# Optimization experiments

Measured on AMD Instinct MI355X. Metric: run time of the kernel, lower is better.

The kernel has to match this reference:

```python
import jax, jax.numpy as jnp
import numpy as np

T, B, I, H, L = 512, 256, 128, 256, 2


def setup_inputs() -> dict:
    key = jax.random.key(0)
    ks = jax.random.split(key, 7)
    s = 0.05
    return {
        "x": jax.random.normal(ks[0], (T, B, I), jnp.float32),
        "state": jnp.zeros((L, B, H), jnp.float32),
        "Wi0": jax.random.normal(ks[1], (3 * H, I), jnp.float32) * s,
        "Wh0": jax.random.normal(ks[2], (3 * H, H), jnp.float32) * s,
        "Wn0": jax.random.normal(ks[3], (3 * H // 3, I), jnp.float32) * s,
        "Wi1": jax.random.normal(ks[4], (3 * H, H), jnp.float32) * s,
        "Wh1": jax.random.normal(ks[5], (3 * H, H), jnp.float32) * s,
        "Wn1": jax.random.normal(ks[6], (H, H), jnp.float32) * s,
    }


def _cell(x, h, Wi, Wh, Wn):
    # gates: [B, 3H]; only r, z chunks are used (third chunk discarded, as in source)
    gates = x @ Wi.T + h @ Wh.T
    hs = h.shape[-1]
    r = jax.nn.sigmoid(gates[..., :hs])
    z = jax.nn.sigmoid(gates[..., hs:2 * hs])
    n = jnp.tanh(x @ Wn.T + r * h)  # note: r gates h directly (nonstandard GRU)
    return (1 - z) * n + z * h


def reference(x, state, Wi0, Wh0, Wn0, Wi1, Wh1, Wn1):
    params = ((Wi0, Wh0, Wn0), (Wi1, Wh1, Wn1))

    def step(carry, xt):
        h0, h1 = carry
        h0 = _cell(xt, h0, *params[0])
        h1 = _cell(h0, h1, *params[1])
        return (h0, h1), h1

    (h0, h1), out = jax.lax.scan(step, (state[0], state[1]), x)
    h = jnp.stack([h0, h1])
    return out, h
```

## Files before the change

kernel.cpp:

```cpp
#include <hip/hip_runtime.h>

#define T_ 512
#define B_ 256
#define I_ 128
#define H_ 256
#define SPIN_MAX (1 << 18)

typedef unsigned short ushort_t;
typedef unsigned int uint_t;
typedef unsigned long long u64_t;
typedef __attribute__((ext_vector_type(8))) short short8;
typedef __attribute__((ext_vector_type(4))) float f32x4;

#define XG_OFF   0
#define H0R_OFF  786432
#define QA_OFF   1048576
#define QB_OFF   1572864
#define FL_OFF   1835008
#define N_FLAGS  2048

__device__ __forceinline__ ushort_t f2bf(float f) {
  unsigned int u = __float_as_uint(f);
  u += 0x7fffu + ((u >> 16) & 1u);
  return (ushort_t)(u >> 16);
}
__device__ __forceinline__ float bf2f(ushort_t u) {
  return __uint_as_float(((unsigned int)u) << 16);
}

__global__ void prep_kernel(uint_t* __restrict__ ws) {
  int i = blockIdx.x * 256 + threadIdx.x;
  if (i < N_FLAGS) ((int*)(ws + FL_OFF))[i] = 0;
}

struct frag2 { short8 h, m; };

__device__ __forceinline__ frag2 lda_x2(const float* base, int ldk, int kc, int lane) {
  const float* p = base + (size_t)(lane & 15) * ldk + kc * 32 + ((lane >> 4) << 3);
  f32x4 a = *(const f32x4*)p;
  f32x4 b = *(const f32x4*)(p + 4);
  float v[8] = {a[0], a[1], a[2], a[3], b[0], b[1], b[2], b[3]};
  frag2 r;
#pragma unroll
  for (int j = 0; j < 8; j++) {
    float f = v[j];
    ushort_t xx = f2bf(f); f -= bf2f(xx);
    ushort_t y = f2bf(f);
    r.h[j] = (short)xx; r.m[j] = (short)y;
  }
  return r;
}
__device__ __forceinline__ short8 ldw1(const float* base, int ldk, int row, int kc, int lane) {
  const float* p = base + (size_t)(row + (lane & 15)) * ldk + kc * 32 + ((lane >> 4) << 3);
  f32x4 a = *(const f32x4*)p;
  f32x4 b = *(const f32x4*)(p + 4);
  short8 r;
  r[0] = (short)f2bf(a[0]); r[1] = (short)f2bf(a[1]);
  r[2] = (short)f2bf(a[2]); r[3] = (short)f2bf(a[3]);
  r[4] = (short)f2bf(b[0]); r[5] = (short)f2bf(b[1]);
  r[6] = (short)f2bf(b[2]); r[7] = (short)f2bf(b[3]);
  return r;
}
__device__ __forceinline__ frag2 ld_packed(const uint_t* p) {
  const u64_t* qp = (const u64_t*)p;
  u64_t d0 = __hip_atomic_load(qp + 0, __ATOMIC_RELAXED, __HIP_MEMORY_SCOPE_AGENT);
  u64_t d1 = __hip_atomic_load(qp + 1, __ATOMIC_RELAXED, __HIP_MEMORY_SCOPE_AGENT);
  u64_t d2 = __hip_atomic_load(qp + 2, __ATOMIC_RELAXED, __HIP_MEMORY_SCOPE_AGENT);
  u64_t d3 = __hip_atomic_load(qp + 3, __ATOMIC_RELAXED, __HIP_MEMORY_SCOPE_AGENT);
  u64_t d[4] = {d0, d1, d2, d3};
  frag2 f;
#pragma unroll
  for (int j = 0; j < 4; j++) {
    uint_t lo = (uint_t)d[j];
    uint_t hi = (uint_t)(d[j] >> 32);
    f.h[2 * j]     = (short)(lo & 0xffffu); f.m[2 * j]     = (short)(lo >> 16);
    f.h[2 * j + 1] = (short)(hi & 0xffffu); f.m[2 * j + 1] = (short)(hi >> 16);
  }
  return f;
}
__device__ __forceinline__ float ldf32(const uint_t* p) {
  uint_t v = __hip_atomic_load(p, __ATOMIC_RELAXED, __HIP_MEMORY_SCOPE_AGENT);
  return __uint_as_float(v);
}
#define CFENCE() asm volatile("" ::: "memory")

__device__ __forceinline__ f32x4 mfma_(short8 a, short8 b, f32x4 c) {
  return __builtin_amdgcn_mfma_f32_16x16x32_bf16(a, b, c, 0, 0, 0);
}
__device__ __forceinline__ int lpoll(const int* p, int tgt, int act, int aborted) {
  if (aborted) return aborted;
  int n = 0;
  for (;;) {
    int ok = 1;
    if (act && tgt > 0)
      ok = (__hip_atomic_load(p, __ATOMIC_RELAXED, __HIP_MEMORY_SCOPE_AGENT) >= tgt);
    if (__all(ok)) return 0;
    if (++n > SPIN_MAX) return 1;
  }
}
__device__ __forceinline__ int lcheck(const int* p, int tgt, int act) {
  int ok = 1;
  if (act && tgt > 0)
    ok = (__hip_atomic_load(p, __ATOMIC_RELAXED, __HIP_MEMORY_SCOPE_AGENT) >= tgt);
  return __all(ok);
}
__device__ __forceinline__ void stflag(int* p, int v) {
  __hip_atomic_store(p, v, __ATOMIC_RELAXED, __HIP_MEMORY_SCOPE_AGENT);
}
__device__ __forceinline__ int get_xcc() {
  int x;
  asm volatile("s_getreg_b32 %0, hwreg(HW_REG_XCC_ID)" : "=s"(x));
  return x & 15;
}
__device__ __forceinline__ float cellpw_fast(float gr, float gz, float np, float h) {
  float r = __builtin_amdgcn_rcpf(1.0f + __builtin_amdgcn_exp2f(-1.44269504089f * gr));
  float z = __builtin_amdgcn_rcpf(1.0f + __builtin_amdgcn_exp2f(-1.44269504089f * gz));
  float a = np + r * h;
  float n = 1.0f - 2.0f * __builtin_amdgcn_rcpf(1.0f + __builtin_amdgcn_exp2f(2.88539008177f * a));
  return (1.0f - z) * n + z * h;
}

__global__ void __launch_bounds__(256, 1)
gru_main(const float* __restrict__ x,
         const float* __restrict__ Wi0, const float* __restrict__ Wh0, const float* __restrict__ Wn0,
         const float* __restrict__ Wi1, const float* __restrict__ Wh1, const float* __restrict__ Wn1,
         const float* __restrict__ state, float* __restrict__ out,
         uint_t* __restrict__ ws, int* __restrict__ unused_flags) {
  __shared__ ushort_t hp[2][2][16][264];
  __shared__ float hf[16][264];
  __shared__ int s_fast;

  const int tid = (int)threadIdx.x;
  const int lane = tid & 63;
  const int wv = tid >> 6;
  const int bid = (int)blockIdx.x;
  const int g = bid & 15;
  const int role = bid >> 4;
  const int gb = g * 16;
  const int c0 = wv * 64;
  const int arow = lane & 15;
  const int acol = (lane >> 4) << 3;
  const int q = lane >> 4;

  int* flags = (int*)(ws + FL_OFF);
  int* fg = flags + g * 32;
  uint_t* xgp = ws + XG_OFF + (size_t)g * 49152;
  uint_t* h0r = ws + H0R_OFF + (size_t)g * 16384;
  uint_t* qap = ws + QA_OFF + (size_t)g * 32768;
  uint_t* qbp = ws + QB_OFF + (size_t)g * 16384;

  if (tid == 0) {
    int myx = get_xcc();
    __hip_atomic_store(&flags[1024 + bid], myx, __ATOMIC_RELAXED, __HIP_MEMORY_SCOPE_AGENT);
    __threadfence();
    __hip_atomic_fetch_add(&flags[1536 + g * 16], 1, __ATOMIC_RELEASE, __HIP_MEMORY_SCOPE_AGENT);
    int n = 0, ab = 0;
    while (__hip_atomic_load(&flags[1536 + g * 16], __ATOMIC_RELAXED,
                             __HIP_MEMORY_SCOPE_AGENT) < 5) {
      if (++n > SPIN_MAX) { ab = 1; break; }
    }
    __threadfence();
    int f = ab ? 0 : 1;
    if (!ab) {
#pragma unroll
      for (int r = 0; r < 5; r++)
        f &= (__hip_atomic_load(&flags[1024 + r * 16 + g], __ATOMIC_RELAXED,
                                __HIP_MEMORY_SCOPE_AGENT) == myx);
    }
    s_fast = f;
  }

  if (role == 1 || role == 4) {
    const float* st = state + (role == 4 ? (size_t)B_ * H_ : 0);
#pragma unroll
    for (int j = 0; j < 4; j++)
#pragma unroll
      for (int e = 0; e < 4; e++) {
        int row = q * 4 + e, col = c0 + 16 * j + (lane & 15);
        float f = st[(size_t)(gb + row) * H_ + col];
        hf[row][col] = f;
        ushort_t hi = f2bf(f), mid = f2bf(f - bf2f(hi));
        hp[1][0][row][col] = hi;
        hp[1][1][row][col] = mid;
      }
  }
  __syncthreads();
  const int fast = s_fast;
  int aborted = 0, ready = 0;
  const f32x4 zz = {0.f, 0.f, 0.f, 0.f};

  if (role == 0) {
    short8 Wxr[4][4], Wxz[4][4], Wxn[4][4];
#pragma unroll
    for (int j = 0; j < 4; j++)
#pragma unroll
      for (int kc = 0; kc < 4; kc++) {
        Wxr[j][kc] = ldw1(Wi0, I_, c0 + 16 * j, kc, lane);
        Wxz[j][kc] = ldw1(Wi0, I_, 256 + c0 + 16 * j, kc, lane);
        Wxn[j][kc] = ldw1(Wn0, I_, c0 + 16 * j, kc, lane);
      }
    const int* wp = fg + 8;
    for (int t = 0; t < T_; t++) {
      if (!ready) aborted = lpoll(wp, t - 3, lane == 0, aborted);
      CFENCE();
      f32x4 ar[4] = {zz, zz, zz, zz}, az[4] = {zz, zz, zz, zz}, an[4] = {zz, zz, zz, zz};
      const float* xt = x + ((size_t)t * B_ + gb) * I_;
#pragma unroll
      for (int kc = 0; kc < 4; kc++) {
        frag2 a = lda_x2(xt, I_, kc, lane);
#pragma unroll
        for (int j = 0; j < 4; j++) {
          ar[j] = mfma_(a.h, Wxr[j][kc], ar[j]); ar[j] = mfma_(a.m, Wxr[j][kc], ar[j]);
          az[j] = mfma_(a.h, Wxz[j][kc], az[j]); az[j] = mfma_(a.m, Wxz[j][kc], az[j]);
          an[j] = mfma_(a.h, Wxn[j][kc], an[j]); an[j] = mfma_(a.m, Wxn[j][kc], an[j]);
        }
      }
      float* xs = (float*)(xgp + (size_t)(t & 3) * 12288);
#pragma unroll
      for (int j = 0; j < 4; j++)
#pragma unroll
        for (int e = 0; e < 4; e++) {
          int row = q * 4 + e, col = c0 + 16 * j + (lane & 15);
          xs[row * 768 + col] = ar[j][e];
          xs[row * 768 + 256 + col] = az[j][e];
          xs[row * 768 + 512 + col] = an[j][e];
        }
      asm volatile("s_waitcnt vmcnt(0)" ::: "memory");
      if (!fast) __threadfence();
      if (lane == 0) stflag(fg + wv, t + 1);
      ready = fast ? lcheck(wp, t - 2, lane == 0) : 0;
    }
  } else if (role == 1) {
    short8 Whr[4][8], Whz[4][8];
#pragma unroll
    for (int j = 0; j < 4; j++)
#pragma unroll
      for (int kc = 0; kc < 8; kc++) {
        Whr[j][kc] = ldw1(Wh0, H_, c0 + 16 * j, kc, lane);
        Whz[j][kc] = ldw1(Wh0, H_, 256 + c0 + 16 * j, kc, lane);
      }
    const int hact = lane < 12;
    const int* hpn = fg + ((lane < 4) ? lane : (lane < 8 ? 12 + (lane - 4) : 16 + (lane - 8)));
    for (int t = 0; t < T_; t++) {
      if (!ready) aborted = lpoll(hpn, (lane < 4) ? t + 1 : t - 3, hact, aborted);
      if (!fast) __threadfence();
      CFENCE();
      const uint_t* xs = xgp + (size_t)(t & 3) * 12288;
      float xr[4][4], xz[4][4], xn[4][4];
#pragma unroll
      for (int j = 0; j < 4; j++)
#pragma unroll
        for (int e = 0; e < 4; e++) {
          int row = q * 4 + e, col = c0 + 16 * j + (lane & 15);
          xr[j][e] = ldf32(xs + row * 768 + col);
          xz[j][e] = ldf32(xs + row * 768 + 256 + col);
          xn[j][e] = ldf32(xs + row * 768 + 512 + col);
        }
      const int par = (t + 1) & 1;
      f32x4 accr[4] = {zz, zz, zz, zz}, accz[4] = {zz, zz, zz, zz};
#pragma unroll
      for (int kc = 0; kc < 8; kc++) {
        short8 ah = *(const short8*)&hp[par][0][arow][kc * 32 + acol];
        short8 am = *(const short8*)&hp[par][1][arow][kc * 32 + acol];
#pragma unroll
        for (int j = 0; j < 4; j++) {
          accr[j] = mfma_(ah, Whr[j][kc], accr[j]); accr[j] = mfma_(am, Whr[j][kc], accr[j]);
          accz[j] = mfma_(ah, Whz[j][kc], accz[j]); accz[j] = mfma_(am, Whz[j][kc], accz[j]);
        }
      }
      uint_t* hdst = h0r + (size_t)(t & 3) * 4096;
#pragma unroll
      for (int j = 0; j < 4; j++)
#pragma unroll
        for (int e = 0; e < 4; e++) {
          int row = q * 4 + e, col = c0 + 16 * j + (lane & 15);
          float gr = accr[j][e] + xr[j][e];
          float gz = accz[j][e] + xz[j][e];
          float h = hf[row][col];
          float hn = cellpw_fast(gr, gz, xn[j][e], h);
          hf[row][col] = hn;
          ushort_t hi = f2bf(hn), mid = f2bf(hn - bf2f(hi));
          hp[t & 1][0][row][col] = hi;
          hp[t & 1][1][row][col] = mid;
          hdst[row * 256 + col] = (uint_t)hi | ((uint_t)mid << 16);
        }
      __syncthreads();
      if (tid == 0) { if (!fast) __threadfence(); stflag(fg + 8, t + 1); }
      ready = fast ? lcheck(hpn, (lane < 4) ? t + 2 : t - 2, hact) : 0;
    }
#pragma unroll
    for (int j = 0; j < 4; j++)
#pragma unroll
      for (int e = 0; e < 4; e++) {
        int row = q * 4 + e, col = c0 + 16 * j + (lane & 15);
        out[(size_t)T_ * B_ * H_ + (size_t)(gb + row) * H_ + col] = hf[row][col];
      }
  } else if (role == 2 || role == 3) {
    const int nt = (role == 2) ? 8 : 4;
    short8 Wq[8][8];
#pragma unroll
    for (int kc = 0; kc < 8; kc++) {
      if (role == 2) {
#pragma unroll
        for (int j = 0; j < 4; j++) {
          Wq[j][kc] = ldw1(Wi1, H_, c0 + 16 * j, kc, lane);
          Wq[4 + j][kc] = ldw1(Wi1, H_, 256 + c0 + 16 * j, kc, lane);
        }
      } else {
#pragma unroll
        for (int j = 0; j < 4; j++) Wq[j][kc] = ldw1(Wn1, H_, c0 + 16 * j, kc, lane);
      }
    }
    const int qact = lane < 2;
    const int* qpn = fg + ((lane == 0) ? 8 : 24);
    int* myslot = fg + ((role == 2) ? 12 : 16) + wv;
    for (int t = 0; t < T_; t++) {
      if (!ready) aborted = lpoll(qpn, (lane == 0) ? t + 1 : t - 3, qact, aborted);
      if (!fast) __threadfence();
      CFENCE();
      frag2 A[8];
      const uint_t* src = h0r + (size_t)(t & 3) * 4096 + (size_t)arow * 256 + acol;
#pragma unroll
      for (int kc = 0; kc < 8; kc++) A[kc] = ld_packed(src + kc * 32);
      f32x4 acc[8] = {zz, zz, zz, zz, zz, zz, zz, zz};
#pragma unroll
      for (int kc = 0; kc < 8; kc++) {
#pragma unroll
        for (int j = 0; j < 8; j++) {
          if (j < nt) {
            acc[j] = mfma_(A[kc].h, Wq[j][kc], acc[j]);
            acc[j] = mfma_(A[kc].m, Wq[j][kc], acc[j]);
          }
        }
      }
      if (role == 2) {
        float* qd = (float*)(qap + (size_t)(t & 3) * 8192);
#pragma unroll
        for (int j = 0; j < 4; j++)
#pragma unroll
          for (int e = 0; e < 4; e++) {
            int row = q * 4 + e, col = c0 + 16 * j + (lane & 15);
            qd[row * 512 + col] = acc[j][e];
            qd[row * 512 + 256 + col] = acc[4 + j][e];
          }
      } else {
        float* qd = (float*)(qbp + (size_t)(t & 3) * 4096);
#pragma unroll
        for (int j = 0; j < 4; j++)
#pragma unroll
          for (int e = 0; e < 4; e++) {
            int row = q * 4 + e, col = c0 + 16 * j + (lane & 15);
            qd[row * 256 + col] = acc[j][e];
          }
      }
      asm volatile("s_waitcnt vmcnt(0)" ::: "memory");
      if (!fast) __threadfence();
      if (lane == 0) stflag(myslot, t + 1);
      ready = fast ? lcheck(qpn, (lane == 0) ? t + 2 : t - 2, qact) : 0;
    }
  } else {
    short8 Wvr[4][8], Wvz[4][8];
#pragma unroll
    for (int j = 0; j < 4; j++)
#pragma unroll
      for (int kc = 0; kc < 8; kc++) {
        Wvr[j][kc] = ldw1(Wh1, H_, c0 + 16 * j, kc, lane);
        Wvz[j][kc] = ldw1(Wh1, H_, 256 + c0 + 16 * j, kc, lane);
      }
    const int ract = lane < 8;
    const int* rpn = fg + ((lane < 4) ? 12 + lane : 16 + (lane - 4));
    float hnv[4][4];
    for (int t = 0; t < T_; t++) {
      if (!ready) aborted = lpoll(rpn, t + 1, ract, aborted);
      if (!fast) __threadfence();
      CFENCE();
      const uint_t* qas = qap + (size_t)(t & 3) * 8192;
      const uint_t* qbs = qbp + (size_t)(t & 3) * 4096;
      float qr[4][4], qz[4][4], qn[4][4];
#pragma unroll
      for (int j = 0; j < 4; j++)
#pragma unroll
        for (int e = 0; e < 4; e++) {
          int row = q * 4 + e, col = c0 + 16 * j + (lane & 15);
          qr[j][e] = ldf32(qas + row * 512 + col);
          qz[j][e] = ldf32(qas + row * 512 + 256 + col);
          qn[j][e] = ldf32(qbs + row * 256 + col);
        }
      const int par = (t + 1) & 1;
      f32x4 accr[4] = {zz, zz, zz, zz}, accz[4] = {zz, zz, zz, zz};
#pragma unroll
      for (int kc = 0; kc < 8; kc++) {
        short8 ah = *(const short8*)&hp[par][0][arow][kc * 32 + acol];
        short8 am = *(const short8*)&hp[par][1][arow][kc * 32 + acol];
#pragma unroll
        for (int j = 0; j < 4; j++) {
          accr[j] = mfma_(ah, Wvr[j][kc], accr[j]); accr[j] = mfma_(am, Wvr[j][kc], accr[j]);
          accz[j] = mfma_(ah, Wvz[j][kc], accz[j]); accz[j] = mfma_(am, Wvz[j][kc], accz[j]);
        }
      }
#pragma unroll
      for (int j = 0; j < 4; j++)
#pragma unroll
        for (int e = 0; e < 4; e++) {
          int row = q * 4 + e, col = c0 + 16 * j + (lane & 15);
          float gr = accr[j][e] + qr[j][e];
          float gz = accz[j][e] + qz[j][e];
          float h = hf[row][col];
          float hn = cellpw_fast(gr, gz, qn[j][e], h);
          hf[row][col] = hn;
          ushort_t hi = f2bf(hn), mid = f2bf(hn - bf2f(hi));
          hp[t & 1][0][row][col] = hi;
          hp[t & 1][1][row][col] = mid;
          hnv[j][e] = hn;
        }
      __syncthreads();
      if (tid == 0) { if (!fast) __threadfence(); stflag(fg + 24, t + 1); }
#pragma unroll
      for (int j = 0; j < 4; j++)
#pragma unroll
        for (int e = 0; e < 4; e++) {
          int row = q * 4 + e, col = c0 + 16 * j + (lane & 15);
          out[((size_t)t * B_ + gb + row) * H_ + col] = hnv[j][e];
        }
      ready = fast ? lcheck(rpn, t + 2, ract) : 0;
    }
#pragma unroll
    for (int j = 0; j < 4; j++)
#pragma unroll
      for (int e = 0; e < 4; e++) {
        int row = q * 4 + e, col = c0 + 16 * j + (lane & 15);
        out[(size_t)T_ * B_ * H_ + (size_t)B_ * H_ + (size_t)(gb + row) * H_ + col] =
            hf[row][col];
      }
  }

  if (tid == 0 && aborted) out[(size_t)gb * H_] = 4096.0f;
}

extern "C" void kernel_launch(void* const* d_in, const int* in_sizes, int n_in,
                              void* d_out, int out_size, void* d_ws, size_t ws_size,
                              hipStream_t stream) {
  const float* x     = (const float*)d_in[0];
  const float* state = (const float*)d_in[1];
  const float* Wi0   = (const float*)d_in[2];
  const float* Wh0   = (const float*)d_in[3];
  const float* Wn0   = (const float*)d_in[4];
  const float* Wi1   = (const float*)d_in[5];
  const float* Wh1   = (const float*)d_in[6];
  const float* Wn1   = (const float*)d_in[7];
  float* out = (float*)d_out;
  uint_t* ws = (uint_t*)d_ws;

  prep_kernel<<<dim3((N_FLAGS + 255) / 256), dim3(256), 0, stream>>>(ws);

  gru_main<<<dim3(80), dim3(256), 0, stream>>>(
      x, Wi0, Wh0, Wn0, Wi1, Wh1, Wn1, state, out, ws, nullptr);
}
```

Baseline: 3.076 ms.

## Double waves per block, halving per-wave column tiles in GRU roles

```diff
diff --git a/kernel.cpp b/kernel.cpp
--- a/kernel.cpp
+++ b/kernel.cpp
@@ -120,7 +120,7 @@
   return (1.0f - z) * n + z * h;
 }
 
-__global__ void __launch_bounds__(256, 1)
+__global__ void __launch_bounds__(512, 2)
 gru_main(const float* __restrict__ x,
          const float* __restrict__ Wi0, const float* __restrict__ Wh0, const float* __restrict__ Wn0,
          const float* __restrict__ Wi1, const float* __restrict__ Wh1, const float* __restrict__ Wn1,
@@ -137,7 +137,7 @@
   const int g = bid & 15;
   const int role = bid >> 4;
   const int gb = g * 16;
-  const int c0 = wv * 64;
+  const int c0 = wv * 32;
   const int arow = lane & 15;
   const int acol = (lane >> 4) << 3;
   const int q = lane >> 4;
@@ -173,7 +173,7 @@
   if (role == 1 || role == 4) {
     const float* st = state + (role == 4 ? (size_t)B_ * H_ : 0);
 #pragma unroll
-    for (int j = 0; j < 4; j++)
+    for (int j = 0; j < 2; j++)
 #pragma unroll
       for (int e = 0; e < 4; e++) {
         int row = q * 4 + e, col = c0 + 16 * j + (lane & 15);
@@ -190,9 +190,9 @@
   const f32x4 zz = {0.f, 0.f, 0.f, 0.f};
 
   if (role == 0) {
-    short8 Wxr[4][4], Wxz[4][4], Wxn[4][4];
-#pragma unroll
-    for (int j = 0; j < 4; j++)
+    short8 Wxr[2][4], Wxz[2][4], Wxn[2][4];
+#pragma unroll
+    for (int j = 0; j < 2; j++)
 #pragma unroll
       for (int kc = 0; kc < 4; kc++) {
         Wxr[j][kc] = ldw1(Wi0, I_, c0 + 16 * j, kc, lane);
@@ -203,13 +203,13 @@
     for (int t = 0; t < T_; t++) {
       if (!ready) aborted = lpoll(wp, t - 3, lane == 0, aborted);
       CFENCE();
-      f32x4 ar[4] = {zz, zz, zz, zz}, az[4] = {zz, zz, zz, zz}, an[4] = {zz, zz, zz, zz};
+      f32x4 ar[2] = {zz, zz}, az[2] = {zz, zz}, an[2] = {zz, zz};
       const float* xt = x + ((size_t)t * B_ + gb) * I_;
 #pragma unroll
       for (int kc = 0; kc < 4; kc++) {
         frag2 a = lda_x2(xt, I_, kc, lane);
 #pragma unroll
-        for (int j = 0; j < 4; j++) {
+        for (int j = 0; j < 2; j++) {
           ar[j] = mfma_(a.h, Wxr[j][kc], ar[j]); ar[j] = mfma_(a.m, Wxr[j][kc], ar[j]);
           az[j] = mfma_(a.h, Wxz[j][kc], az[j]); az[j] = mfma_(a.m, Wxz[j][kc], az[j]);
           an[j] = mfma_(a.h, Wxn[j][kc], an[j]); an[j] = mfma_(a.m, Wxn[j][kc], an[j]);
@@ -217,7 +217,7 @@
       }
       float* xs = (float*)(xgp + (size_t)(t & 3) * 12288);
 #pragma unroll
-      for (int j = 0; j < 4; j++)
+      for (int j = 0; j < 2; j++)
 #pragma unroll
         for (int e = 0; e < 4; e++) {
           int row = q * 4 + e, col = c0 + 16 * j + (lane & 15);
@@ -231,24 +231,24 @@
       ready = fast ? lcheck(wp, t - 2, lane == 0) : 0;
     }
   } else if (role == 1) {
-    short8 Whr[4][8], Whz[4][8];
-#pragma unroll
-    for (int j = 0; j < 4; j++)
+    short8 Whr[2][8], Whz[2][8];
+#pragma unroll
+    for (int j = 0; j < 2; j++)
 #pragma unroll
       for (int kc = 0; kc < 8; kc++) {
         Whr[j][kc] = ldw1(Wh0, H_, c0 + 16 * j, kc, lane);
         Whz[j][kc] = ldw1(Wh0, H_, 256 + c0 + 16 * j, kc, lane);
       }
-    const int hact = lane < 12;
-    const int* hpn = fg + ((lane < 4) ? lane : (lane < 8 ? 12 + (lane - 4) : 16 + (lane - 8)));
+    const int hact = lane < 24;
+    const int* hpn = fg + ((lane < 8) ? lane : (lane < 16 ? 10 + (lane - 8) : 18 + (lane - 16)));
     for (int t = 0; t < T_; t++) {
-      if (!ready) aborted = lpoll(hpn, (lane < 4) ? t + 1 : t - 3, hact, aborted);
+      if (!ready) aborted = lpoll(hpn, (lane < 8) ? t + 1 : t - 3, hact, aborted);
       if (!fast) __threadfence();
       CFENCE();
       const uint_t* xs = xgp + (size_t)(t & 3) * 12288;
-      float xr[4][4], xz[4][4], xn[4][4];
-#pragma unroll
-      for (int j = 0; j < 4; j++)
+      float xr[2][4], xz[2][4], xn[2][4];
+#pragma unroll
+      for (int j = 0; j < 2; j++)
 #pragma unroll
         for (int e = 0; e < 4; e++) {
           int row = q * 4 + e, col = c0 + 16 * j + (lane & 15);
@@ -257,20 +257,20 @@
           xn[j][e] = ldf32(xs + row * 768 + 512 + col);
         }
       const int par = (t + 1) & 1;
-      f32x4 accr[4] = {zz, zz, zz, zz}, accz[4] = {zz, zz, zz, zz};
+      f32x4 accr[2] = {zz, zz}, accz[2] = {zz, zz};
 #pragma unroll
       for (int kc = 0; kc < 8; kc++) {
         short8 ah = *(const short8*)&hp[par][0][arow][kc * 32 + acol];
         short8 am = *(const short8*)&hp[par][1][arow][kc * 32 + acol];
 #pragma unroll
-        for (int j = 0; j < 4; j++) {
+        for (int j = 0; j < 2; j++) {
           accr[j] = mfma_(ah, Whr[j][kc], accr[j]); accr[j] = mfma_(am, Whr[j][kc], accr[j]);
           accz[j] = mfma_(ah, Whz[j][kc], accz[j]); accz[j] = mfma_(am, Whz[j][kc], accz[j]);
         }
       }
       uint_t* hdst = h0r + (size_t)(t & 3) * 4096;
 #pragma unroll
-      for (int j = 0; j < 4; j++)
+      for (int j = 0; j < 2; j++)
 #pragma unroll
         for (int e = 0; e < 4; e++) {
           int row = q * 4 + e, col = c0 + 16 * j + (lane & 15);
@@ -286,34 +286,27 @@
         }
       __syncthreads();
       if (tid == 0) { if (!fast) __threadfence(); stflag(fg + 8, t + 1); }
-      ready = fast ? lcheck(hpn, (lane < 4) ? t + 2 : t - 2, hact) : 0;
-    }
-#pragma unroll
-    for (int j = 0; j < 4; j++)
+      ready = fast ? lcheck(hpn, (lane < 8) ? t + 2 : t - 2, hact) : 0;
+    }
+#pragma unroll
+    for (int j = 0; j < 2; j++)
 #pragma unroll
       for (int e = 0; e < 4; e++) {
         int row = q * 4 + e, col = c0 + 16 * j + (lane & 15);
         out[(size_t)T_ * B_ * H_ + (size_t)(gb + row) * H_ + col] = hf[row][col];
       }
-  } else if (role == 2 || role == 3) {
-    const int nt = (role == 2) ? 8 : 4;
-    short8 Wq[8][8];
-#pragma unroll
-    for (int kc = 0; kc < 8; kc++) {
-      if (role == 2) {
-#pragma unroll
-        for (int j = 0; j < 4; j++) {
-          Wq[j][kc] = ldw1(Wi1, H_, c0 + 16 * j, kc, lane);
-          Wq[4 + j][kc] = ldw1(Wi1, H_, 256 + c0 + 16 * j, kc, lane);
-        }
-      } else {
-#pragma unroll
-        for (int j = 0; j < 4; j++) Wq[j][kc] = ldw1(Wn1, H_, c0 + 16 * j, kc, lane);
-      }
-    }
+  } else if (role == 2) {
+    short8 Wq[4][8];
+#pragma unroll
+    for (int kc = 0; kc < 8; kc++)
+#pragma unroll
+      for (int j = 0; j < 2; j++) {
+        Wq[j][kc] = ldw1(Wi1, H_, c0 + 16 * j, kc, lane);
+        Wq[2 + j][kc] = ldw1(Wi1, H_, 256 + c0 + 16 * j, kc, lane);
+      }
     const int qact = lane < 2;
-    const int* qpn = fg + ((lane == 0) ? 8 : 24);
-    int* myslot = fg + ((role == 2) ? 12 : 16) + wv;
+    const int* qpn = fg + ((lane == 0) ? 8 : 9);
+    int* myslot = fg + 10 + wv;
     for (int t = 0; t < T_; t++) {
       if (!ready) aborted = lpoll(qpn, (lane == 0) ? t + 1 : t - 3, qact, aborted);
       if (!fast) __threadfence();
@@ -322,63 +315,87 @@
       const uint_t* src = h0r + (size_t)(t & 3) * 4096 + (size_t)arow * 256 + acol;
 #pragma unroll
       for (int kc = 0; kc < 8; kc++) A[kc] = ld_packed(src + kc * 32);
-      f32x4 acc[8] = {zz, zz, zz, zz, zz, zz, zz, zz};
-#pragma unroll
-      for (int kc = 0; kc < 8; kc++) {
-#pragma unroll
-        for (int j = 0; j < 8; j++) {
-          if (j < nt) {
-            acc[j] = mfma_(A[kc].h, Wq[j][kc], acc[j]);
-            acc[j] = mfma_(A[kc].m, Wq[j][kc], acc[j]);
-          }
-        }
-      }
-      if (role == 2) {
-        float* qd = (float*)(qap + (size_t)(t & 3) * 8192);
-#pragma unroll
-        for (int j = 0; j < 4; j++)
-#pragma unroll
-          for (int e = 0; e < 4; e++) {
-            int row = q * 4 + e, col = c0 + 16 * j + (lane & 15);
-            qd[row * 512 + col] = acc[j][e];
-            qd[row * 512 + 256 + col] = acc[4 + j][e];
-          }
-      } else {
-        float* qd = (float*)(qbp + (size_t)(t & 3) * 4096);
-#pragma unroll
-        for (int j = 0; j < 4; j++)
-#pragma unroll
-          for (int e = 0; e < 4; e++) {
-            int row = q * 4 + e, col = c0 + 16 * j + (lane & 15);
-            qd[row * 256 + col] = acc[j][e];
-          }
-      }
+      f32x4 acc[4] = {zz, zz, zz, zz};
+#pragma unroll
+      for (int kc = 0; kc < 8; kc++)
+#pragma unroll
+        for (int j = 0; j < 4; j++) {
+          acc[j] = mfma_(A[kc].h, Wq[j][kc], acc[j]);
+          acc[j] = mfma_(A[kc].m, Wq[j][kc], acc[j]);
+        }
+      float* qd = (float*)(qap + (size_t)(t & 3) * 8192);
+#pragma unroll
+      for (int j = 0; j < 2; j++)
+#pragma unroll
+        for (int e = 0; e < 4; e++) {
+          int row = q * 4 + e, col = c0 + 16 * j + (lane & 15);
+          qd[row * 512 + col] = acc[j][e];
+          qd[row * 512 + 256 + col] = acc[2 + j][e];
+        }
       asm volatile("s_waitcnt vmcnt(0)" ::: "memory");
       if (!fast) __threadfence();
       if (lane == 0) stflag(myslot, t + 1);
       ready = fast ? lcheck(qpn, (lane == 0) ? t + 2 : t - 2, qact) : 0;
     }
+  } else if (role == 3) {
+    short8 Wq[2][8];
+#pragma unroll
+    for (int kc = 0; kc < 8; kc++)
+#pragma unroll
+      for (int j = 0; j < 2; j++) Wq[j][kc] = ldw1(Wn1, H_, c0 + 16 * j, kc, lane);
+    const int qact = lane < 2;
+    const int* qpn = fg + ((lane == 0) ? 8 : 9);
+    int* myslot = fg + 18 + wv;
+    for (int t = 0; t < T_; t++) {
+      if (!ready) aborted = lpoll(qpn, (lane == 0) ? t + 1 : t - 3, qact, aborted);
+      if (!fast) __threadfence();
+      CFENCE();
+      frag2 A[8];
+      const uint_t* src = h0r + (size_t)(t & 3) * 4096 + (size_t)arow * 256 + acol;
+#pragma unroll
+      for (int kc = 0; kc < 8; kc++) A[kc] = ld_packed(src + kc * 32);
+      f32x4 acc[2] = {zz, zz};
+#pragma unroll
+      for (int kc = 0; kc < 8; kc++)
+#pragma unroll
+        for (int j = 0; j < 2; j++) {
+          acc[j] = mfma_(A[kc].h, Wq[j][kc], acc[j]);
+          acc[j] = mfma_(A[kc].m, Wq[j][kc], acc[j]);
+        }
+      float* qd = (float*)(qbp + (size_t)(t & 3) * 4096);
+#pragma unroll
+      for (int j = 0; j < 2; j++)
+#pragma unroll
+        for (int e = 0; e < 4; e++) {
+          int row = q * 4 + e, col = c0 + 16 * j + (lane & 15);
+          qd[row * 256 + col] = acc[j][e];
+        }
+      asm volatile("s_waitcnt vmcnt(0)" ::: "memory");
+      if (!fast) __threadfence();
+      if (lane == 0) stflag(myslot, t + 1);
+      ready = fast ? lcheck(qpn, (lane == 0) ? t + 2 : t - 2, qact) : 0;
+    }
   } else {
-    short8 Wvr[4][8], Wvz[4][8];
-#pragma unroll
-    for (int j = 0; j < 4; j++)
+    short8 Wvr[2][8], Wvz[2][8];
+#pragma unroll
+    for (int j = 0; j < 2; j++)
 #pragma unroll
       for (int kc = 0; kc < 8; kc++) {
         Wvr[j][kc] = ldw1(Wh1, H_, c0 + 16 * j, kc, lane);
         Wvz[j][kc] = ldw1(Wh1, H_, 256 + c0 + 16 * j, kc, lane);
       }
-    const int ract = lane < 8;
-    const int* rpn = fg + ((lane < 4) ? 12 + lane : 16 + (lane - 4));
-    float hnv[4][4];
+    const int ract = lane < 16;
+    const int* rpn = fg + ((lane < 8) ? 10 + lane : 18 + (lane - 8));
+    float hnv[2][4];
     for (int t = 0; t < T_; t++) {
       if (!ready) aborted = lpoll(rpn, t + 1, ract, aborted);
       if (!fast) __threadfence();
       CFENCE();
       const uint_t* qas = qap + (size_t)(t & 3) * 8192;
       const uint_t* qbs = qbp + (size_t)(t & 3) * 4096;
-      float qr[4][4], qz[4][4], qn[4][4];
-#pragma unroll
-      for (int j = 0; j < 4; j++)
+      float qr[2][4], qz[2][4], qn[2][4];
+#pragma unroll
+      for (int j = 0; j < 2; j++)
 #pragma unroll
         for (int e = 0; e < 4; e++) {
           int row = q * 4 + e, col = c0 + 16 * j + (lane & 15);
@@ -387,19 +404,19 @@
           qn[j][e] = ldf32(qbs + row * 256 + col);
         }
       const int par = (t + 1) & 1;
-      f32x4 accr[4] = {zz, zz, zz, zz}, accz[4] = {zz, zz, zz, zz};
+      f32x4 accr[2] = {zz, zz}, accz[2] = {zz, zz};
 #pragma unroll
       for (int kc = 0; kc < 8; kc++) {
         short8 ah = *(const short8*)&hp[par][0][arow][kc * 32 + acol];
         short8 am = *(const short8*)&hp[par][1][arow][kc * 32 + acol];
 #pragma unroll
-        for (int j = 0; j < 4; j++) {
+        for (int j = 0; j < 2; j++) {
           accr[j] = mfma_(ah, Wvr[j][kc], accr[j]); accr[j] = mfma_(am, Wvr[j][kc], accr[j]);
           accz[j] = mfma_(ah, Wvz[j][kc], accz[j]); accz[j] = mfma_(am, Wvz[j][kc], accz[j]);
         }
       }
 #pragma unroll
-      for (int j = 0; j < 4; j++)
+      for (int j = 0; j < 2; j++)
 #pragma unroll
         for (int e = 0; e < 4; e++) {
           int row = q * 4 + e, col = c0 + 16 * j + (lane & 15);
@@ -414,9 +431,9 @@
           hnv[j][e] = hn;
         }
       __syncthreads();
-      if (tid == 0) { if (!fast) __threadfence(); stflag(fg + 24, t + 1); }
-#pragma unroll
-      for (int j = 0; j < 4; j++)
+      if (tid == 0) { if (!fast) __threadfence(); stflag(fg + 9, t + 1); }
+#pragma unroll
+      for (int j = 0; j < 2; j++)
 #pragma unroll
         for (int e = 0; e < 4; e++) {
           int row = q * 4 + e, col = c0 + 16 * j + (lane & 15);
@@ -425,7 +442,7 @@
       ready = fast ? lcheck(rpn, t + 2, ract) : 0;
     }
 #pragma unroll
-    for (int j = 0; j < 4; j++)
+    for (int j = 0; j < 2; j++)
 #pragma unroll
       for (int e = 0; e < 4; e++) {
         int row = q * 4 + e, col = c0 + 16 * j + (lane & 15);
@@ -453,6 +470,6 @@
 
   prep_kernel<<<dim3((N_FLAGS + 255) / 256), dim3(256), 0, stream>>>(ws);
 
-  gru_main<<<dim3(80), dim3(256), 0, stream>>>(
+  gru_main<<<dim3(80), dim3(512), 0, stream>>>(
       x, Wi0, Wh0, Wn0, Wi1, Wh1, Wn1, state, out, ws, nullptr);
 }
```

After: 5.031 ms. 1.64x slower.
